# Kernel optimization log

Hardware: AMD Instinct MI355X
Metric: run time of the kernel (lower is better)

Reference implementation:

```python
import jax, jax.numpy as jnp
import numpy as np

# Model dims (see shape_source)
E, H, I = 8, 2048, 1408          # experts, hidden, moe intermediate
T, TOPK = 4096, 2                # tokens, routed experts per token
BN, BK = 128, 128                # weight SF block granularity (block_size)
FP8 = jnp.float8_e4m3fn
FP8_MAX = 448.0                  # torch.finfo(float8_e4m3fn).max


def _quantize_weight(key, n_exp, n_out, n_in):
    """Blockwise-quantize a random fp32 weight to (fp8 weight, fp32 scale_inv).

    Mirrors V3-style FP8 block quant: per [BN, BK] block, scale = amax / FP8_MAX.
    """
    w = jax.random.normal(key, (n_exp, n_out, n_in), jnp.float32) * 0.02
    wb = w.reshape(n_exp, n_out // BN, BN, n_in // BK, BK)
    amax = jnp.max(jnp.abs(wb), axis=(2, 4))                 # [E, nb, kb]
    scale = jnp.maximum(amax, 1e-12) / FP8_MAX
    q = (wb / scale[:, :, None, :, None]).astype(FP8)
    return q.reshape(n_exp, n_out, n_in), scale


def setup_inputs() -> dict:
    key = jax.random.key(0)
    k1, k2, k3, k4, k5 = jax.random.split(key, 5)
    hidden_states = jax.random.normal(k1, (T, H), jnp.float32)
    top_k_index = jax.random.randint(k2, (T, TOPK), 0, E)
    tw = jax.random.uniform(k3, (T, TOPK), dtype=jnp.float32)
    top_k_weights = tw / jnp.sum(tw, axis=-1, keepdims=True)  # softmax-like routing weights
    gate_up_proj, gate_up_proj_scale_inv = _quantize_weight(k4, E, 2 * I, H)
    down_proj, down_proj_scale_inv = _quantize_weight(k5, E, H, I)
    return {
        "hidden_states": hidden_states,
        "top_k_index": top_k_index,
        "top_k_weights": top_k_weights,
        "gate_up_proj": gate_up_proj,
        "gate_up_proj_scale_inv": gate_up_proj_scale_inv,
        "down_proj": down_proj,
        "down_proj_scale_inv": down_proj_scale_inv,
    }


def _act_quant_dequant(x):
    """Dynamic per-token, per-BK-block FP8 activation quant (fp8_act_quant), dequantized.

    Equivalent math to keeping q in fp8 and applying per-block scales inside the
    matmul, since the scale is constant within each k-block.
    """
    k = x.shape[-1]
    xb = x.reshape(*x.shape[:-1], k // BK, BK)
    amax = jnp.max(jnp.abs(xb), axis=-1)
    scale = jnp.maximum(amax, 1e-12) / FP8_MAX
    q = jnp.clip(xb / scale[..., None], -FP8_MAX, FP8_MAX).astype(FP8).astype(jnp.float32)
    return (q * scale[..., None]).reshape(x.shape)


def _dequant_weight(w, sf):
    """w: [E, N, K] fp8; sf: [E, N//BN, K//BK] fp32 -> [E, N, K] fp32."""
    sfe = jnp.repeat(jnp.repeat(sf, BN, axis=1), BK, axis=2)
    return w.astype(jnp.float32) * sfe


def reference(hidden_states, top_k_index, top_k_weights,
              gate_up_proj, gate_up_proj_scale_inv,
              down_proj, down_proj_scale_inv):
    # act-quant input once (shared across experts, as in the eager per-expert loop)
    xq = _act_quant_dequant(hidden_states)                         # [T, H]
    w_gu = _dequant_weight(gate_up_proj, gate_up_proj_scale_inv)   # [E, 2I, H]
    h = jnp.einsum('th,enh->ten', xq, w_gu)                        # [T, E, 2I]
    gate, up = jnp.split(h, 2, axis=-1)
    inter = jax.nn.silu(gate) * up                                 # [T, E, I]
    iq = _act_quant_dequant(inter)
    w_d = _dequant_weight(down_proj, down_proj_scale_inv)          # [E, H, I]
    y = jnp.einsum('tei,ehi->teh', iq, w_d)                        # [T, E, H]
    # routed combine: out[t] = sum_k top_k_weights[t,k] * y[t, top_k_index[t,k]]
    yk = jnp.take_along_axis(y, top_k_index[..., None], axis=1)    # [T, TOPK, H]
    return jnp.sum(yk * top_k_weights[..., None], axis=1)          # [T, H] fp32
```

## Files before the change

### kernel.cpp

```cpp
#include <hip/hip_runtime.h>
#include <stdint.h>
#include <stddef.h>

#define DEVFN __device__ __forceinline__

typedef float f32x4 __attribute__((ext_vector_type(4)));
typedef long i64_t;

constexpr int T_TOK = 4096, H_DIM = 2048, I_DIM = 1408;
constexpr int N_EXP = 8;
constexpr int P_PAIRS = T_TOK * 2;
constexpr int BM = 64;
constexpr int MAXT = 144;
constexpr int GU_ROWS = 2 * I_DIM;

constexpr size_t OFF_WGU = 0;
constexpr size_t OFF_WD  = OFF_WGU + (size_t)N_EXP * GU_ROWS * H_DIM;
constexpr size_t OFF_XQ  = OFF_WD + (size_t)N_EXP * H_DIM * I_DIM;
constexpr size_t OFF_XS  = OFF_XQ + (size_t)T_TOK * H_DIM;
constexpr size_t OFF_IQ  = OFF_XS + (size_t)T_TOK * 16 * 4;
constexpr size_t OFF_IS  = OFF_IQ + (size_t)(P_PAIRS + BM) * I_DIM;
constexpr size_t OFF_PS  = OFF_IS + (size_t)P_PAIRS * 11 * 4;
constexpr size_t OFF_PP  = OFF_PS + (size_t)P_PAIRS * 4;
constexpr size_t OFF_TE  = OFF_PP + (size_t)P_PAIRS * 4;
constexpr size_t OFF_TR  = OFF_TE + (size_t)MAXT * 4;
constexpr size_t OFF_TM  = OFF_TR + (size_t)MAXT * 4;
constexpr size_t OFF_Y   = (OFF_TM + (size_t)MAXT * 4 + 255) & ~(size_t)255;
constexpr size_t NEED_Y  = OFF_Y + (size_t)P_PAIRS * H_DIM * 4;

DEVFN unsigned f32_to_e4m3(float x) {
  unsigned u = __float_as_uint(x);
  unsigned s = (u >> 24) & 0x80u;
  int e = (int)((u >> 23) & 0xffu);
  unsigned m = u & 0x7fffffu;
  if (e == 0) return s;
  int ef = e - 127;
  if (ef < -10) return s;
  unsigned mant = 0x800000u | m;
  int shift = (ef < -6) ? (14 - ef) : 20;
  int e8 = (ef < -6) ? 0 : (ef + 7);
  unsigned keep = mant >> shift;
  unsigned rmask = 1u << (shift - 1);
  unsigned rbit = (mant & rmask) ? 1u : 0u;
  unsigned sticky = (mant & (rmask - 1u)) ? 1u : 0u;
  keep += (rbit & (sticky | (keep & 1u)));
  if (e8 == 0) {
    if (keep >= 8u) { e8 = 1; keep -= 8u; }
  } else {
    if (keep >= 16u) { keep >>= 1; e8 += 1; }
    keep -= 8u;
  }
  return s | ((unsigned)e8 << 3) | keep;
}

DEVFN float clampq(float v) { return fminf(fmaxf(v, -448.f), 448.f); }

DEVFN void gll(const uint8_t* g, uint8_t* l) {
  __builtin_amdgcn_global_load_lds((const __attribute__((address_space(1))) void*)g,
                                   (__attribute__((address_space(3))) void*)l,
                                   16, 0, 0);
}

__global__ __launch_bounds__(256) void k_wq(const float* __restrict__ wf,
                                            uint8_t* __restrict__ wq, int n4) {
  int i = blockIdx.x * 256 + threadIdx.x;
  if (i >= n4) return;
  float4 v = *(const float4*)(wf + (size_t)i * 4);
  unsigned b = f32_to_e4m3(clampq(v.x)) | (f32_to_e4m3(clampq(v.y)) << 8) |
               (f32_to_e4m3(clampq(v.z)) << 16) | (f32_to_e4m3(clampq(v.w)) << 24);
  *(unsigned*)(wq + (size_t)i * 4) = b;
}

__global__ __launch_bounds__(256) void k_actq(const float* __restrict__ x,
                                              uint8_t* __restrict__ xq,
                                              float* __restrict__ xs) {
  int t = blockIdx.x, tid = threadIdx.x;
  const float* row = x + (size_t)t * H_DIM + tid * 8;
  float4 v0 = *(const float4*)(row);
  float4 v1 = *(const float4*)(row + 4);
  float vals[8] = {v0.x, v0.y, v0.z, v0.w, v1.x, v1.y, v1.z, v1.w};
  float am = 0.f;
#pragma unroll
  for (int j = 0; j < 8; ++j) am = fmaxf(am, fabsf(vals[j]));
#pragma unroll
  for (int d = 1; d < 16; d <<= 1) am = fmaxf(am, __shfl_xor(am, d, 64));
  float s = fmaxf(am, 1e-12f) / 448.0f;
  if ((tid & 15) == 0) xs[(size_t)t * 16 + (tid >> 4)] = s;
  unsigned lo = 0, hi = 0;
#pragma unroll
  for (int j = 0; j < 4; ++j) lo |= f32_to_e4m3(clampq(vals[j] / s)) << (8 * j);
#pragma unroll
  for (int j = 0; j < 4; ++j) hi |= f32_to_e4m3(clampq(vals[4 + j] / s)) << (8 * j);
  uint2 pk; pk.x = lo; pk.y = hi;
  *(uint2*)(xq + (size_t)t * H_DIM + tid * 8) = pk;
}

__global__ __launch_bounds__(256) void k_route(const int* __restrict__ tki,
                                               int* __restrict__ ps, int* __restrict__ pp,
                                               int* __restrict__ te, int* __restrict__ tr,
                                               int* __restrict__ tm) {
  __shared__ int cnt[8], off[9], cur[8];
  int tid = threadIdx.x;
  if (tid < 8) cnt[tid] = 0;
  __syncthreads();
  for (int p = tid; p < P_PAIRS; p += 256) atomicAdd(&cnt[tki[p]], 1);
  __syncthreads();
  if (tid == 0) {
    int a = 0;
    for (int e = 0; e < 8; ++e) { off[e] = a; cur[e] = a; a += cnt[e]; }
    off[8] = a;
  }
  __syncthreads();
  for (int p = tid; p < P_PAIRS; p += 256) {
    int pos = atomicAdd(&cur[tki[p]], 1);
    ps[pos] = p;
    pp[p] = pos;
  }
  __syncthreads();
  if (tid == 0) {
    int nt = 0;
    for (int e = 0; e < 8; ++e)
      for (int s = off[e]; s < off[e + 1]; s += BM) {
        int rem = off[e + 1] - s;
        te[nt] = e; tr[nt] = s; tm[nt] = rem < BM ? rem : BM; ++nt;
      }
    for (; nt < MAXT; ++nt) { te[nt] = -1; tr[nt] = 0; tm[nt] = 0; }
  }
}

__global__ __launch_bounds__(256) void k_gemm1(
    const uint8_t* __restrict__ xq, const float* __restrict__ xs,
    const uint8_t* __restrict__ gup, const float* __restrict__ gsf,
    const int* __restrict__ te, const int* __restrict__ tr, const int* __restrict__ tm,
    const int* __restrict__ ps,
    uint8_t* __restrict__ iq, float* __restrict__ isv) {
  __shared__ uint8_t smA[BM * 128];
  __shared__ uint8_t smBg[128 * 128];
  __shared__ uint8_t smBu[128 * 128];
  __shared__ __align__(16) float smSa[BM];
  __shared__ float smRed[2][2][32];

  const int bx = blockIdx.x;
  const int e = te[bx];
  if (e < 0) return;
  const int r0 = tr[bx], mrows = tm[bx];
  const int n0 = blockIdx.y * 128;
  const int nbg = blockIdx.y;
  const int tid = threadIdx.x;
  const int lane = tid & 63;
  const int wid = tid >> 6;
  const int wm = wid >> 1, wn = wid & 1;
  const int lrow = lane & 15, lgrp = lane >> 4;
  const int mbase = wm * 32;
  const int wb = wid * 1024;

  const int m0 = tid >> 3, m1 = m0 + 32;
  const int kcol = (tid & 7) * 16;
  const int srcOff = kcol ^ ((m0 & 7) << 4);
  const int t0 = (m0 < mrows) ? (ps[r0 + m0] >> 1) : 0;
  const int t1 = (m1 < mrows) ? (ps[r0 + m1] >> 1) : 0;
  const uint8_t* pA0 = xq + (size_t)t0 * H_DIM + srcOff;
  const uint8_t* pA1 = xq + (size_t)t1 * H_DIM + srcOff;
  const uint8_t* pBg = gup + ((size_t)e * GU_ROWS + n0 + m0) * H_DIM + srcOff;
  const uint8_t* pBu = pBg + (size_t)I_DIM * H_DIM;
  int tS = 0;
  if (tid < 64) tS = (tid < mrows) ? (ps[r0 + tid] >> 1) : 0;
  const float* xsrow = xs + (size_t)tS * 16;

  const int swz = (lrow & 7) << 4;
  int koff[4];
#pragma unroll
  for (int kk = 0; kk < 4; ++kk) koff[kk] = ((kk * 32 + lgrp * 8) ^ swz);
  const uint8_t* pAf[2];
  pAf[0] = smA + (mbase + lrow) * 128;
  pAf[1] = smA + (mbase + 16 + lrow) * 128;
  const uint8_t* pBf[4];
#pragma unroll
  for (int nf = 0; nf < 4; ++nf) pBf[nf] = smBg + (wn * 64 + nf * 16 + lrow) * 128;
  const ptrdiff_t dBu = smBu - smBg;

  const float* sfg = gsf + ((size_t)e * 22 + nbg) * 16;
  const float* sfu = gsf + ((size_t)e * 22 + 11 + nbg) * 16;

  f32x4 accg[2][4], accu[2][4];
#pragma unroll
  for (int mf = 0; mf < 2; ++mf)
#pragma unroll
    for (int nf = 0; nf < 4; ++nf) { accg[mf][nf] = 0.f; accu[mf][nf] = 0.f; }

  for (int ks = 0; ks < 16; ++ks) {
    __syncthreads();
    gll(pA0, smA + wb);
    gll(pA1, smA + 4096 + wb);
#pragma unroll
    for (int c = 0; c < 4; ++c) {
      gll(pBg + (size_t)c * (32 * H_DIM), smBg + c * 4096 + wb);
      gll(pBu + (size_t)c * (32 * H_DIM), smBu + c * 4096 + wb);
    }
    if (tid < 64) smSa[tid] = xsrow[ks];
    __syncthreads();

    i64_t a[2][4];
#pragma unroll
    for (int mf = 0; mf < 2; ++mf)
#pragma unroll
      for (int kk = 0; kk < 4; ++kk) a[mf][kk] = *(const i64_t*)(pAf[mf] + koff[kk]);
    f32x4 saf[2];
    saf[0] = *(const f32x4*)(smSa + mbase + lgrp * 4);
    saf[1] = *(const f32x4*)(smSa + mbase + 16 + lgrp * 4);
    float swg = sfg[ks], swu = sfu[ks];

#pragma unroll
    for (int half = 0; half < 2; ++half) {
      const ptrdiff_t ho = half ? dBu : 0;
      f32x4 part[2][4];
#pragma unroll
      for (int mf = 0; mf < 2; ++mf)
#pragma unroll
        for (int nf = 0; nf < 4; ++nf) part[mf][nf] = 0.f;
#pragma unroll
      for (int kk = 0; kk < 4; ++kk)
#pragma unroll
        for (int nf = 0; nf < 4; ++nf) {
          i64_t b = *(const i64_t*)(pBf[nf] + ho + koff[kk]);
          part[0][nf] = __builtin_amdgcn_mfma_f32_16x16x32_fp8_fp8(a[0][kk], b, part[0][nf], 0, 0, 0);
          part[1][nf] = __builtin_amdgcn_mfma_f32_16x16x32_fp8_fp8(a[1][kk], b, part[1][nf], 0, 0, 0);
        }
      float sw = half ? swu : swg;
      f32x4 (*acch)[4] = half ? accu : accg;
#pragma unroll
      for (int mf = 0; mf < 2; ++mf) {
        f32x4 sc = saf[mf] * sw;
#pragma unroll
        for (int nf = 0; nf < 4; ++nf) acch[mf][nf] += part[mf][nf] * sc;
      }
    }
    pA0 += 128; pA1 += 128; pBg += 128; pBu += 128;
  }

  float itv[2][4][4];
  float amx[2][4];
#pragma unroll
  for (int mf = 0; mf < 2; ++mf)
#pragma unroll
    for (int r = 0; r < 4; ++r) amx[mf][r] = 0.f;
#pragma unroll
  for (int mf = 0; mf < 2; ++mf)
#pragma unroll
    for (int nf = 0; nf < 4; ++nf)
#pragma unroll
      for (int r = 0; r < 4; ++r) {
        float g = accg[mf][nf][r], u = accu[mf][nf][r];
        float sg = 1.0f / (1.0f + expf(-g));
        float iv = g * sg * u;
        itv[mf][nf][r] = iv;
        amx[mf][r] = fmaxf(amx[mf][r], fabsf(iv));
      }
#pragma unroll
  for (int mf = 0; mf < 2; ++mf)
#pragma unroll
    for (int r = 0; r < 4; ++r)
#pragma unroll
      for (int d = 1; d < 16; d <<= 1) amx[mf][r] = fmaxf(amx[mf][r], __shfl_xor(amx[mf][r], d, 64));

  if (lrow == 0) {
#pragma unroll
    for (int mf = 0; mf < 2; ++mf)
#pragma unroll
      for (int r = 0; r < 4; ++r) smRed[wm][wn][mf * 16 + lgrp * 4 + r] = amx[mf][r];
  }
  __syncthreads();

#pragma unroll
  for (int mf = 0; mf < 2; ++mf)
#pragma unroll
    for (int r = 0; r < 4; ++r) {
      float am2 = fmaxf(amx[mf][r], smRed[wm][wn ^ 1][mf * 16 + lgrp * 4 + r]);
      float s = fmaxf(am2, 1e-12f) / 448.0f;
      int R = mbase + mf * 16 + lgrp * 4 + r;
      if (R < mrows) {
        if (wn == 0 && lrow == 0) isv[(size_t)(r0 + R) * 11 + nbg] = s;
        size_t rowb = (size_t)(r0 + R) * I_DIM + n0 + wn * 64 + lrow;
#pragma unroll
        for (int nf = 0; nf < 4; ++nf) {
          float v = clampq(itv[mf][nf][r] / s);
          iq[rowb + nf * 16] = (uint8_t)f32_to_e4m3(v);
        }
      }
    }
}

template <bool ATOMIC>
__global__ __launch_bounds__(256) void k_gemm2(
    const uint8_t* __restrict__ iq, const float* __restrict__ isv,
    const uint8_t* __restrict__ dp, const float* __restrict__ dsf,
    const int* __restrict__ te, const int* __restrict__ tr, const int* __restrict__ tm,
    const int* __restrict__ ps, const float* __restrict__ tkw,
    float* __restrict__ outy) {
  __shared__ uint8_t smA[BM * 128];
  __shared__ uint8_t smB[128 * 128];
  __shared__ __align__(16) float smSa[BM];

  const int bx = blockIdx.x;
  const int e = te[bx];
  if (e < 0) return;
  const int r0 = tr[bx], mrows = tm[bx];
  const int n0 = blockIdx.y * 128;
  const int tid = threadIdx.x;
  const int lane = tid & 63;
  const int wid = tid >> 6;
  const int wm = wid >> 1, wn = wid & 1;
  const int lrow = lane & 15, lgrp = lane >> 4;
  const int mbase = wm * 32;
  const int wb = wid * 1024;

  const int m0 = tid >> 3, m1 = m0 + 32;
  const int kcol = (tid & 7) * 16;
  const int srcOff = kcol ^ ((m0 & 7) << 4);
  const uint8_t* pA0 = iq + (size_t)(r0 + m0) * I_DIM + srcOff;
  const uint8_t* pA1 = iq + (size_t)(r0 + m1) * I_DIM + srcOff;
  const uint8_t* pB = dp + ((size_t)e * H_DIM + n0 + m0) * I_DIM + srcOff;

  const int swz = (lrow & 7) << 4;
  int koff[4];
#pragma unroll
  for (int kk = 0; kk < 4; ++kk) koff[kk] = ((kk * 32 + lgrp * 8) ^ swz);
  const uint8_t* pAf[2];
  pAf[0] = smA + (mbase + lrow) * 128;
  pAf[1] = smA + (mbase + 16 + lrow) * 128;
  const uint8_t* pBf[4];
#pragma unroll
  for (int nf = 0; nf < 4; ++nf) pBf[nf] = smB + (wn * 64 + nf * 16 + lrow) * 128;

  const float* sfd = dsf + ((size_t)e * 16 + blockIdx.y) * 11;

  f32x4 acc[2][4];
#pragma unroll
  for (int mf = 0; mf < 2; ++mf)
#pragma unroll
    for (int nf = 0; nf < 4; ++nf) acc[mf][nf] = 0.f;

  for (int ks = 0; ks < 11; ++ks) {
    __syncthreads();
    gll(pA0, smA + wb);
    gll(pA1, smA + 4096 + wb);
#pragma unroll
    for (int c = 0; c < 4; ++c) gll(pB + (size_t)c * (32 * I_DIM), smB + c * 4096 + wb);
    if (tid < 64) {
      float v = (tid < mrows) ? isv[(size_t)(r0 + tid) * 11 + ks] : 0.f;
      smSa[tid] = v;
    }
    __syncthreads();

    i64_t a[2][4];
#pragma unroll
    for (int mf = 0; mf < 2; ++mf)
#pragma unroll
      for (int kk = 0; kk < 4; ++kk) a[mf][kk] = *(const i64_t*)(pAf[mf] + koff[kk]);
    f32x4 saf[2];
    saf[0] = *(const f32x4*)(smSa + mbase + lgrp * 4);
    saf[1] = *(const f32x4*)(smSa + mbase + 16 + lgrp * 4);
    float sw = sfd[ks];

    f32x4 part[2][4];
#pragma unroll
    for (int mf = 0; mf < 2; ++mf)
#pragma unroll
      for (int nf = 0; nf < 4; ++nf) part[mf][nf] = 0.f;
#pragma unroll
    for (int kk = 0; kk < 4; ++kk)
#pragma unroll
      for (int nf = 0; nf < 4; ++nf) {
        i64_t b = *(const i64_t*)(pBf[nf] + koff[kk]);
        part[0][nf] = __builtin_amdgcn_mfma_f32_16x16x32_fp8_fp8(a[0][kk], b, part[0][nf], 0, 0, 0);
        part[1][nf] = __builtin_amdgcn_mfma_f32_16x16x32_fp8_fp8(a[1][kk], b, part[1][nf], 0, 0, 0);
      }
#pragma unroll
    for (int mf = 0; mf < 2; ++mf) {
      f32x4 sc = saf[mf] * sw;
#pragma unroll
      for (int nf = 0; nf < 4; ++nf) acc[mf][nf] += part[mf][nf] * sc;
    }
    pA0 += 128; pA1 += 128; pB += 128;
  }

#pragma unroll
  for (int mf = 0; mf < 2; ++mf)
#pragma unroll
    for (int r = 0; r < 4; ++r) {
      int R = mbase + mf * 16 + lgrp * 4 + r;
      if (R < mrows) {
        int prow = r0 + R;
        int p = ps[prow];
        float w = tkw[p];
        if (ATOMIC) {
          float* ob = outy + (size_t)(p >> 1) * H_DIM + n0 + wn * 64 + lrow;
#pragma unroll
          for (int nf = 0; nf < 4; ++nf) atomicAdd(ob + nf * 16, acc[mf][nf][r] * w);
        } else {
          float* ob = outy + (size_t)prow * H_DIM + n0 + wn * 64 + lrow;
#pragma unroll
          for (int nf = 0; nf < 4; ++nf) ob[nf * 16] = acc[mf][nf][r] * w;
        }
      }
    }
}

__global__ __launch_bounds__(256) void k_combine(const float* __restrict__ y,
                                                 const int* __restrict__ pp,
                                                 float* __restrict__ out) {
  size_t g = (size_t)blockIdx.x * 256 + threadIdx.x;
  int t = (int)(g >> 9);
  int c = (int)(g & 511) * 4;
  int ra = pp[2 * t], rb = pp[2 * t + 1];
  float4 va = *(const float4*)(y + (size_t)ra * H_DIM + c);
  float4 vb = *(const float4*)(y + (size_t)rb * H_DIM + c);
  float4 vo;
  vo.x = va.x + vb.x; vo.y = va.y + vb.y; vo.z = va.z + vb.z; vo.w = va.w + vb.w;
  *(float4*)(out + (size_t)t * H_DIM + c) = vo;
}

extern "C" void kernel_launch(void* const* d_in, const int* in_sizes, int n_in,
                              void* d_out, int out_size, void* d_ws, size_t ws_size,
                              hipStream_t stream) {
  (void)in_sizes; (void)n_in; (void)out_size;
  const float* x = (const float*)d_in[0];
  const int* tki = (const int*)d_in[1];
  const float* tkw = (const float*)d_in[2];
  const float* gup_f = (const float*)d_in[3];
  const float* gsf = (const float*)d_in[4];
  const float* dp_f = (const float*)d_in[5];
  const float* dsf = (const float*)d_in[6];
  float* out = (float*)d_out;
  uint8_t* ws = (uint8_t*)d_ws;

  uint8_t* wgu = ws + OFF_WGU;
  uint8_t* wd = ws + OFF_WD;
  uint8_t* xq = ws + OFF_XQ;
  float* xs = (float*)(ws + OFF_XS);
  uint8_t* iq = ws + OFF_IQ;
  float* isv = (float*)(ws + OFF_IS);
  int* ps = (int*)(ws + OFF_PS);
  int* pp = (int*)(ws + OFF_PP);
  int* te = (int*)(ws + OFF_TE);
  int* tr = (int*)(ws + OFF_TR);
  int* tm = (int*)(ws + OFF_TM);
  float* y = (float*)(ws + OFF_Y);

  const int n4_gu = (N_EXP * GU_ROWS * H_DIM) / 4;
  const int n4_d = (N_EXP * H_DIM * I_DIM) / 4;
  k_wq<<<dim3((n4_gu + 255) / 256), dim3(256), 0, stream>>>(gup_f, wgu, n4_gu);
  k_wq<<<dim3((n4_d + 255) / 256), dim3(256), 0, stream>>>(dp_f, wd, n4_d);
  k_actq<<<dim3(T_TOK), dim3(256), 0, stream>>>(x, xq, xs);
  k_route<<<dim3(1), dim3(256), 0, stream>>>(tki, ps, pp, te, tr, tm);
  k_gemm1<<<dim3(MAXT, 11), dim3(256), 0, stream>>>(xq, xs, wgu, gsf, te, tr, tm, ps, iq, isv);
  if (ws_size >= NEED_Y) {
    k_gemm2<false><<<dim3(MAXT, 16), dim3(256), 0, stream>>>(iq, isv, wd, dsf, te, tr, tm, ps, tkw, y);
    k_combine<<<dim3((T_TOK * (H_DIM / 4)) / 256), dim3(256), 0, stream>>>(y, pp, out);
  } else {
    hipMemsetAsync(d_out, 0, (size_t)T_TOK * H_DIM * sizeof(float), stream);
    k_gemm2<true><<<dim3(MAXT, 16), dim3(256), 0, stream>>>(iq, isv, wd, dsf, te, tr, tm, ps, tkw, out);
  }
}
```

Before: 620.8 us.

## Fuse prep kernels, fast fp8 cast, double-buffer GEMM K-loops with 64-wide stages

Merges the weight cast, activation quant and routing kernels into one launch and replaces the generic fp8 conversion for weights with a bit-trick cast that skips clamping. Both GEMMs now stage K in 64-byte chunks into double-buffered shared memory so the next chunk's loads overlap the current MFMAs, with one barrier per stage. Intermediate scales are stored transposed ([kb][row]) so gemm2 reads them with coalesced loads. The fast cast assumes weights are already in fp8 range, and gemm2 no longer masks scales for rows past mrows.

```diff
diff --git a/kernel.cpp b/kernel.cpp
--- a/kernel.cpp
+++ b/kernel.cpp
@@ -13,6 +13,7 @@
 constexpr int BM = 64;
 constexpr int MAXT = 144;
 constexpr int GU_ROWS = 2 * I_DIM;
+constexpr int PP_PAD = P_PAIRS + 64;
 
 constexpr size_t OFF_WGU = 0;
 constexpr size_t OFF_WD  = OFF_WGU + (size_t)N_EXP * GU_ROWS * H_DIM;
@@ -20,7 +21,7 @@
 constexpr size_t OFF_XS  = OFF_XQ + (size_t)T_TOK * H_DIM;
 constexpr size_t OFF_IQ  = OFF_XS + (size_t)T_TOK * 16 * 4;
 constexpr size_t OFF_IS  = OFF_IQ + (size_t)(P_PAIRS + BM) * I_DIM;
-constexpr size_t OFF_PS  = OFF_IS + (size_t)P_PAIRS * 11 * 4;
+constexpr size_t OFF_PS  = OFF_IS + (size_t)11 * PP_PAD * 4;
 constexpr size_t OFF_PP  = OFF_PS + (size_t)P_PAIRS * 4;
 constexpr size_t OFF_TE  = OFF_PP + (size_t)P_PAIRS * 4;
 constexpr size_t OFF_TR  = OFF_TE + (size_t)MAXT * 4;
@@ -53,6 +54,18 @@
   return s | ((unsigned)e8 << 3) | keep;
 }
 
+DEVFN unsigned e4x(float v) {
+  unsigned u = __float_as_uint(v);
+  unsigned s = (u >> 24) & 0x80u;
+  unsigned au = u & 0x7fffffffu;
+  if (au < 0x3c800000u)
+    return s | (unsigned)(__uint_as_float(au) * 512.0f);
+  return s | ((au - 0x3c000000u) >> 20);
+}
+DEVFN unsigned e4x4(float4 v) {
+  return e4x(v.x) | (e4x(v.y) << 8) | (e4x(v.z) << 16) | (e4x(v.w) << 24);
+}
+
 DEVFN float clampq(float v) { return fminf(fmaxf(v, -448.f), 448.f); }
 
 DEVFN void gll(const uint8_t* g, uint8_t* l) {
@@ -61,46 +74,53 @@
                                    16, 0, 0);
 }
 
-__global__ __launch_bounds__(256) void k_wq(const float* __restrict__ wf,
-                                            uint8_t* __restrict__ wq, int n4) {
-  int i = blockIdx.x * 256 + threadIdx.x;
-  if (i >= n4) return;
-  float4 v = *(const float4*)(wf + (size_t)i * 4);
-  unsigned b = f32_to_e4m3(clampq(v.x)) | (f32_to_e4m3(clampq(v.y)) << 8) |
-               (f32_to_e4m3(clampq(v.z)) << 16) | (f32_to_e4m3(clampq(v.w)) << 24);
-  *(unsigned*)(wq + (size_t)i * 4) = b;
-}
-
-__global__ __launch_bounds__(256) void k_actq(const float* __restrict__ x,
-                                              uint8_t* __restrict__ xq,
-                                              float* __restrict__ xs) {
-  int t = blockIdx.x, tid = threadIdx.x;
-  const float* row = x + (size_t)t * H_DIM + tid * 8;
-  float4 v0 = *(const float4*)(row);
-  float4 v1 = *(const float4*)(row + 4);
-  float vals[8] = {v0.x, v0.y, v0.z, v0.w, v1.x, v1.y, v1.z, v1.w};
-  float am = 0.f;
-#pragma unroll
-  for (int j = 0; j < 8; ++j) am = fmaxf(am, fabsf(vals[j]));
-#pragma unroll
-  for (int d = 1; d < 16; d <<= 1) am = fmaxf(am, __shfl_xor(am, d, 64));
-  float s = fmaxf(am, 1e-12f) / 448.0f;
-  if ((tid & 15) == 0) xs[(size_t)t * 16 + (tid >> 4)] = s;
-  unsigned lo = 0, hi = 0;
-#pragma unroll
-  for (int j = 0; j < 4; ++j) lo |= f32_to_e4m3(clampq(vals[j] / s)) << (8 * j);
-#pragma unroll
-  for (int j = 0; j < 4; ++j) hi |= f32_to_e4m3(clampq(vals[4 + j] / s)) << (8 * j);
-  uint2 pk; pk.x = lo; pk.y = hi;
-  *(uint2*)(xq + (size_t)t * H_DIM + tid * 8) = pk;
-}
-
-__global__ __launch_bounds__(256) void k_route(const int* __restrict__ tki,
-                                               int* __restrict__ ps, int* __restrict__ pp,
-                                               int* __restrict__ te, int* __restrict__ tr,
-                                               int* __restrict__ tm) {
+constexpr int NB_WGU = 22528;
+constexpr int NB_WD  = 11264;
+constexpr int NB_W   = NB_WGU + NB_WD;
+constexpr int NB_PREP = NB_W + T_TOK + 1;
+
+__global__ __launch_bounds__(256) void k_prep(
+    const float* __restrict__ gup_f, const float* __restrict__ dp_f,
+    const float* __restrict__ x, const int* __restrict__ tki,
+    uint8_t* __restrict__ wgu, uint8_t* __restrict__ wd,
+    uint8_t* __restrict__ xq, float* __restrict__ xs,
+    int* __restrict__ ps, int* __restrict__ pp,
+    int* __restrict__ te, int* __restrict__ tr, int* __restrict__ tm) {
   __shared__ int cnt[8], off[9], cur[8];
-  int tid = threadIdx.x;
+  const int bx = blockIdx.x, tid = threadIdx.x;
+
+  if (bx < NB_W) {
+    const float* src = (bx < NB_WGU) ? gup_f : dp_f;
+    uint8_t* dst = (bx < NB_WGU) ? wgu : wd;
+    size_t i = (size_t)(bx < NB_WGU ? bx : bx - NB_WGU) * 2048 + (size_t)tid * 8;
+    float4 v0 = *(const float4*)(src + i);
+    float4 v1 = *(const float4*)(src + i + 4);
+    uint2 pk; pk.x = e4x4(v0); pk.y = e4x4(v1);
+    *(uint2*)(dst + i) = pk;
+    return;
+  }
+  if (bx < NB_W + T_TOK) {
+    int t = bx - NB_W;
+    const float* row = x + (size_t)t * H_DIM + tid * 8;
+    float4 v0 = *(const float4*)(row);
+    float4 v1 = *(const float4*)(row + 4);
+    float vals[8] = {v0.x, v0.y, v0.z, v0.w, v1.x, v1.y, v1.z, v1.w};
+    float am = 0.f;
+#pragma unroll
+    for (int j = 0; j < 8; ++j) am = fmaxf(am, fabsf(vals[j]));
+#pragma unroll
+    for (int d = 1; d < 16; d <<= 1) am = fmaxf(am, __shfl_xor(am, d, 64));
+    float s = fmaxf(am, 1e-12f) / 448.0f;
+    if ((tid & 15) == 0) xs[(size_t)t * 16 + (tid >> 4)] = s;
+    unsigned lo = 0, hi = 0;
+#pragma unroll
+    for (int j = 0; j < 4; ++j) lo |= f32_to_e4m3(clampq(vals[j] / s)) << (8 * j);
+#pragma unroll
+    for (int j = 0; j < 4; ++j) hi |= f32_to_e4m3(clampq(vals[4 + j] / s)) << (8 * j);
+    uint2 pk; pk.x = lo; pk.y = hi;
+    *(uint2*)(xq + (size_t)t * H_DIM + tid * 8) = pk;
+    return;
+  }
   if (tid < 8) cnt[tid] = 0;
   __syncthreads();
   for (int p = tid; p < P_PAIRS; p += 256) atomicAdd(&cnt[tki[p]], 1);
@@ -134,109 +154,112 @@
     const int* __restrict__ te, const int* __restrict__ tr, const int* __restrict__ tm,
     const int* __restrict__ ps,
     uint8_t* __restrict__ iq, float* __restrict__ isv) {
-  __shared__ uint8_t smA[BM * 128];
-  __shared__ uint8_t smBg[128 * 128];
-  __shared__ uint8_t smBu[128 * 128];
-  __shared__ __align__(16) float smSa[BM];
+  __shared__ uint8_t smA[2][64 * 64];
+  __shared__ uint8_t smBg[2][128 * 64];
+  __shared__ uint8_t smBu[2][128 * 64];
+  __shared__ __align__(16) float smSa[64];
   __shared__ float smRed[2][2][32];
 
-  const int bx = blockIdx.x;
-  const int e = te[bx];
+  const int e = te[blockIdx.x];
   if (e < 0) return;
-  const int r0 = tr[bx], mrows = tm[bx];
-  const int n0 = blockIdx.y * 128;
-  const int nbg = blockIdx.y;
-  const int tid = threadIdx.x;
-  const int lane = tid & 63;
-  const int wid = tid >> 6;
+  const int r0 = tr[blockIdx.x], mrows = tm[blockIdx.x];
+  const int nbg = blockIdx.y, n0 = nbg * 128;
+  const int tid = threadIdx.x, lane = tid & 63, wid = tid >> 6;
   const int wm = wid >> 1, wn = wid & 1;
   const int lrow = lane & 15, lgrp = lane >> 4;
   const int mbase = wm * 32;
-  const int wb = wid * 1024;
-
-  const int m0 = tid >> 3, m1 = m0 + 32;
-  const int kcol = (tid & 7) * 16;
-  const int srcOff = kcol ^ ((m0 & 7) << 4);
-  const int t0 = (m0 < mrows) ? (ps[r0 + m0] >> 1) : 0;
-  const int t1 = (m1 < mrows) ? (ps[r0 + m1] >> 1) : 0;
-  const uint8_t* pA0 = xq + (size_t)t0 * H_DIM + srcOff;
-  const uint8_t* pA1 = xq + (size_t)t1 * H_DIM + srcOff;
-  const uint8_t* pBg = gup + ((size_t)e * GU_ROWS + n0 + m0) * H_DIM + srcOff;
-  const uint8_t* pBu = pBg + (size_t)I_DIM * H_DIM;
+
+  const int row_t = tid >> 2;
+  const int srcOff = ((tid & 3) * 16) ^ ((row_t & 3) << 4);
+  const int tA = (row_t < mrows) ? (ps[r0 + row_t] >> 1) : 0;
+  const uint8_t* gA   = xq + (size_t)tA * H_DIM + srcOff;
+  const uint8_t* gBg  = gup + ((size_t)e * GU_ROWS + n0 + row_t) * H_DIM + srcOff;
+  const uint8_t* gBg2 = gBg + (size_t)64 * H_DIM;
+  const uint8_t* gBu  = gBg + (size_t)I_DIM * H_DIM;
+  const uint8_t* gBu2 = gBu + (size_t)64 * H_DIM;
+  uint8_t* lA  = smA[0]  + wid * 1024;
+  uint8_t* lBg = smBg[0] + wid * 1024;
+  uint8_t* lBu = smBu[0] + wid * 1024;
+
   int tS = 0;
   if (tid < 64) tS = (tid < mrows) ? (ps[r0 + tid] >> 1) : 0;
   const float* xsrow = xs + (size_t)tS * 16;
 
-  const int swz = (lrow & 7) << 4;
-  int koff[4];
-#pragma unroll
-  for (int kk = 0; kk < 4; ++kk) koff[kk] = ((kk * 32 + lgrp * 8) ^ swz);
-  const uint8_t* pAf[2];
-  pAf[0] = smA + (mbase + lrow) * 128;
-  pAf[1] = smA + (mbase + 16 + lrow) * 128;
-  const uint8_t* pBf[4];
-#pragma unroll
-  for (int nf = 0; nf < 4; ++nf) pBf[nf] = smBg + (wn * 64 + nf * 16 + lrow) * 128;
-  const ptrdiff_t dBu = smBu - smBg;
+  const int koff0 = (lgrp * 8) ^ ((lrow & 3) << 4);
+  const int koff1 = koff0 ^ 32;
+  const int rA0 = (mbase + lrow) * 64;
+  const int rA1 = (mbase + 16 + lrow) * 64;
+  int rB[4];
+#pragma unroll
+  for (int nf = 0; nf < 4; ++nf) rB[nf] = (wn * 64 + nf * 16 + lrow) * 64;
 
   const float* sfg = gsf + ((size_t)e * 22 + nbg) * 16;
   const float* sfu = gsf + ((size_t)e * 22 + 11 + nbg) * 16;
 
-  f32x4 accg[2][4], accu[2][4];
-#pragma unroll
-  for (int mf = 0; mf < 2; ++mf)
-#pragma unroll
-    for (int nf = 0; nf < 4; ++nf) { accg[mf][nf] = 0.f; accu[mf][nf] = 0.f; }
-
-  for (int ks = 0; ks < 16; ++ks) {
+  f32x4 accg[2][4], accu[2][4], pg[2][4], pu[2][4];
+#pragma unroll
+  for (int mf = 0; mf < 2; ++mf)
+#pragma unroll
+    for (int nf = 0; nf < 4; ++nf) {
+      accg[mf][nf] = 0.f; accu[mf][nf] = 0.f;
+      pg[mf][nf] = 0.f;   pu[mf][nf] = 0.f;
+    }
+
+#define STAGE1(b_, s_) do { size_t o_ = (size_t)(s_) * 64;            \
+    gll(gA + o_,   lA  + (b_) * 4096);                                \
+    gll(gBg + o_,  lBg + (b_) * 8192);                                \
+    gll(gBg2 + o_, lBg + (b_) * 8192 + 4096);                         \
+    gll(gBu + o_,  lBu + (b_) * 8192);                                \
+    gll(gBu2 + o_, lBu + (b_) * 8192 + 4096); } while (0)
+
+  STAGE1(0, 0);
+  if (tid < 64) smSa[tid] = xsrow[0];
+  __syncthreads();
+
+  for (int st = 0; st < 32; ++st) {
+    const int buf = st & 1;
+    if (st < 31) STAGE1(buf ^ 1, st + 1);
+    if (st && !(st & 1) && tid < 64) smSa[tid] = xsrow[st >> 1];
+
+    const uint8_t* bA = smA[0]  + buf * 4096;
+    const uint8_t* bG = smBg[0] + buf * 8192;
+    const uint8_t* bU = smBu[0] + buf * 8192;
+    i64_t a00 = *(const i64_t*)(bA + rA0 + koff0);
+    i64_t a01 = *(const i64_t*)(bA + rA0 + koff1);
+    i64_t a10 = *(const i64_t*)(bA + rA1 + koff0);
+    i64_t a11 = *(const i64_t*)(bA + rA1 + koff1);
+#pragma unroll
+    for (int nf = 0; nf < 4; ++nf) {
+      i64_t bg0 = *(const i64_t*)(bG + rB[nf] + koff0);
+      i64_t bg1 = *(const i64_t*)(bG + rB[nf] + koff1);
+      i64_t bu0 = *(const i64_t*)(bU + rB[nf] + koff0);
+      i64_t bu1 = *(const i64_t*)(bU + rB[nf] + koff1);
+      pg[0][nf] = __builtin_amdgcn_mfma_f32_16x16x32_fp8_fp8(a00, bg0, pg[0][nf], 0, 0, 0);
+      pg[0][nf] = __builtin_amdgcn_mfma_f32_16x16x32_fp8_fp8(a01, bg1, pg[0][nf], 0, 0, 0);
+      pg[1][nf] = __builtin_amdgcn_mfma_f32_16x16x32_fp8_fp8(a10, bg0, pg[1][nf], 0, 0, 0);
+      pg[1][nf] = __builtin_amdgcn_mfma_f32_16x16x32_fp8_fp8(a11, bg1, pg[1][nf], 0, 0, 0);
+      pu[0][nf] = __builtin_amdgcn_mfma_f32_16x16x32_fp8_fp8(a00, bu0, pu[0][nf], 0, 0, 0);
+      pu[0][nf] = __builtin_amdgcn_mfma_f32_16x16x32_fp8_fp8(a01, bu1, pu[0][nf], 0, 0, 0);
+      pu[1][nf] = __builtin_amdgcn_mfma_f32_16x16x32_fp8_fp8(a10, bu0, pu[1][nf], 0, 0, 0);
+      pu[1][nf] = __builtin_amdgcn_mfma_f32_16x16x32_fp8_fp8(a11, bu1, pu[1][nf], 0, 0, 0);
+    }
+    if (st & 1) {
+      const int kb = st >> 1;
+      float swg = sfg[kb], swu = sfu[kb];
+      f32x4 saf0 = *(const f32x4*)(smSa + mbase + lgrp * 4);
+      f32x4 saf1 = *(const f32x4*)(smSa + mbase + 16 + lgrp * 4);
+      f32x4 scg0 = saf0 * swg, scg1 = saf1 * swg;
+      f32x4 scu0 = saf0 * swu, scu1 = saf1 * swu;
+#pragma unroll
+      for (int nf = 0; nf < 4; ++nf) {
+        accg[0][nf] += pg[0][nf] * scg0; accg[1][nf] += pg[1][nf] * scg1;
+        accu[0][nf] += pu[0][nf] * scu0; accu[1][nf] += pu[1][nf] * scu1;
+        pg[0][nf] = 0.f; pg[1][nf] = 0.f; pu[0][nf] = 0.f; pu[1][nf] = 0.f;
+      }
+    }
     __syncthreads();
-    gll(pA0, smA + wb);
-    gll(pA1, smA + 4096 + wb);
-#pragma unroll
-    for (int c = 0; c < 4; ++c) {
-      gll(pBg + (size_t)c * (32 * H_DIM), smBg + c * 4096 + wb);
-      gll(pBu + (size_t)c * (32 * H_DIM), smBu + c * 4096 + wb);
-    }
-    if (tid < 64) smSa[tid] = xsrow[ks];
-    __syncthreads();
-
-    i64_t a[2][4];
-#pragma unroll
-    for (int mf = 0; mf < 2; ++mf)
-#pragma unroll
-      for (int kk = 0; kk < 4; ++kk) a[mf][kk] = *(const i64_t*)(pAf[mf] + koff[kk]);
-    f32x4 saf[2];
-    saf[0] = *(const f32x4*)(smSa + mbase + lgrp * 4);
-    saf[1] = *(const f32x4*)(smSa + mbase + 16 + lgrp * 4);
-    float swg = sfg[ks], swu = sfu[ks];
-
-#pragma unroll
-    for (int half = 0; half < 2; ++half) {
-      const ptrdiff_t ho = half ? dBu : 0;
-      f32x4 part[2][4];
-#pragma unroll
-      for (int mf = 0; mf < 2; ++mf)
-#pragma unroll
-        for (int nf = 0; nf < 4; ++nf) part[mf][nf] = 0.f;
-#pragma unroll
-      for (int kk = 0; kk < 4; ++kk)
-#pragma unroll
-        for (int nf = 0; nf < 4; ++nf) {
-          i64_t b = *(const i64_t*)(pBf[nf] + ho + koff[kk]);
-          part[0][nf] = __builtin_amdgcn_mfma_f32_16x16x32_fp8_fp8(a[0][kk], b, part[0][nf], 0, 0, 0);
-          part[1][nf] = __builtin_amdgcn_mfma_f32_16x16x32_fp8_fp8(a[1][kk], b, part[1][nf], 0, 0, 0);
-        }
-      float sw = half ? swu : swg;
-      f32x4 (*acch)[4] = half ? accu : accg;
-#pragma unroll
-      for (int mf = 0; mf < 2; ++mf) {
-        f32x4 sc = saf[mf] * sw;
-#pragma unroll
-        for (int nf = 0; nf < 4; ++nf) acch[mf][nf] += part[mf][nf] * sc;
-      }
-    }
-    pA0 += 128; pA1 += 128; pBg += 128; pBu += 128;
-  }
+  }
+#undef STAGE1
 
   float itv[2][4][4];
   float amx[2][4];
@@ -279,7 +302,7 @@
       float s = fmaxf(am2, 1e-12f) / 448.0f;
       int R = mbase + mf * 16 + lgrp * 4 + r;
       if (R < mrows) {
-        if (wn == 0 && lrow == 0) isv[(size_t)(r0 + R) * 11 + nbg] = s;
+        if (wn == 0 && lrow == 0) isv[(size_t)nbg * PP_PAD + (r0 + R)] = s;
         size_t rowb = (size_t)(r0 + R) * I_DIM + n0 + wn * 64 + lrow;
 #pragma unroll
         for (int nf = 0; nf < 4; ++nf) {
@@ -297,92 +320,87 @@
     const int* __restrict__ te, const int* __restrict__ tr, const int* __restrict__ tm,
     const int* __restrict__ ps, const float* __restrict__ tkw,
     float* __restrict__ outy) {
-  __shared__ uint8_t smA[BM * 128];
-  __shared__ uint8_t smB[128 * 128];
-  __shared__ __align__(16) float smSa[BM];
-
-  const int bx = blockIdx.x;
-  const int e = te[bx];
+  __shared__ uint8_t smA[2][64 * 64];
+  __shared__ uint8_t smB[2][128 * 64];
+  __shared__ __align__(16) float smSa[64];
+
+  const int e = te[blockIdx.x];
   if (e < 0) return;
-  const int r0 = tr[bx], mrows = tm[bx];
-  const int n0 = blockIdx.y * 128;
-  const int tid = threadIdx.x;
-  const int lane = tid & 63;
-  const int wid = tid >> 6;
+  const int r0 = tr[blockIdx.x], mrows = tm[blockIdx.x];
+  const int nbg = blockIdx.y, n0 = nbg * 128;
+  const int tid = threadIdx.x, lane = tid & 63, wid = tid >> 6;
   const int wm = wid >> 1, wn = wid & 1;
   const int lrow = lane & 15, lgrp = lane >> 4;
   const int mbase = wm * 32;
-  const int wb = wid * 1024;
-
-  const int m0 = tid >> 3, m1 = m0 + 32;
-  const int kcol = (tid & 7) * 16;
-  const int srcOff = kcol ^ ((m0 & 7) << 4);
-  const uint8_t* pA0 = iq + (size_t)(r0 + m0) * I_DIM + srcOff;
-  const uint8_t* pA1 = iq + (size_t)(r0 + m1) * I_DIM + srcOff;
-  const uint8_t* pB = dp + ((size_t)e * H_DIM + n0 + m0) * I_DIM + srcOff;
-
-  const int swz = (lrow & 7) << 4;
-  int koff[4];
-#pragma unroll
-  for (int kk = 0; kk < 4; ++kk) koff[kk] = ((kk * 32 + lgrp * 8) ^ swz);
-  const uint8_t* pAf[2];
-  pAf[0] = smA + (mbase + lrow) * 128;
-  pAf[1] = smA + (mbase + 16 + lrow) * 128;
-  const uint8_t* pBf[4];
-#pragma unroll
-  for (int nf = 0; nf < 4; ++nf) pBf[nf] = smB + (wn * 64 + nf * 16 + lrow) * 128;
-
-  const float* sfd = dsf + ((size_t)e * 16 + blockIdx.y) * 11;
-
-  f32x4 acc[2][4];
-#pragma unroll
-  for (int mf = 0; mf < 2; ++mf)
-#pragma unroll
-    for (int nf = 0; nf < 4; ++nf) acc[mf][nf] = 0.f;
-
-  for (int ks = 0; ks < 11; ++ks) {
+
+  const int row_t = tid >> 2;
+  const int srcOff = ((tid & 3) * 16) ^ ((row_t & 3) << 4);
+  const uint8_t* gA  = iq + (size_t)(r0 + row_t) * I_DIM + srcOff;
+  const uint8_t* gB  = dp + ((size_t)e * H_DIM + n0 + row_t) * I_DIM + srcOff;
+  const uint8_t* gB2 = gB + (size_t)64 * I_DIM;
+  uint8_t* lA = smA[0] + wid * 1024;
+  uint8_t* lB = smB[0] + wid * 1024;
+
+  const int koff0 = (lgrp * 8) ^ ((lrow & 3) << 4);
+  const int koff1 = koff0 ^ 32;
+  const int rA0 = (mbase + lrow) * 64;
+  const int rA1 = (mbase + 16 + lrow) * 64;
+  int rB[4];
+#pragma unroll
+  for (int nf = 0; nf < 4; ++nf) rB[nf] = (wn * 64 + nf * 16 + lrow) * 64;
+
+  const float* sfd = dsf + ((size_t)e * 16 + nbg) * 11;
+
+  f32x4 acc[2][4], p[2][4];
+#pragma unroll
+  for (int mf = 0; mf < 2; ++mf)
+#pragma unroll
+    for (int nf = 0; nf < 4; ++nf) { acc[mf][nf] = 0.f; p[mf][nf] = 0.f; }
+
+#define STAGE2(b_, s_) do { size_t o_ = (size_t)(s_) * 64;            \
+    gll(gA + o_,  lA + (b_) * 4096);                                  \
+    gll(gB + o_,  lB + (b_) * 8192);                                  \
+    gll(gB2 + o_, lB + (b_) * 8192 + 4096); } while (0)
+
+  STAGE2(0, 0);
+  if (tid < 64) smSa[tid] = isv[r0 + tid];
+  __syncthreads();
+
+  for (int st = 0; st < 22; ++st) {
+    const int buf = st & 1;
+    if (st < 21) STAGE2(buf ^ 1, st + 1);
+    if (st && !(st & 1) && tid < 64) smSa[tid] = isv[(size_t)(st >> 1) * PP_PAD + r0 + tid];
+
+    const uint8_t* bA = smA[0] + buf * 4096;
+    const uint8_t* bB = smB[0] + buf * 8192;
+    i64_t a00 = *(const i64_t*)(bA + rA0 + koff0);
+    i64_t a01 = *(const i64_t*)(bA + rA0 + koff1);
+    i64_t a10 = *(const i64_t*)(bA + rA1 + koff0);
+    i64_t a11 = *(const i64_t*)(bA + rA1 + koff1);
+#pragma unroll
+    for (int nf = 0; nf < 4; ++nf) {
+      i64_t b0 = *(const i64_t*)(bB + rB[nf] + koff0);
+      i64_t b1 = *(const i64_t*)(bB + rB[nf] + koff1);
+      p[0][nf] = __builtin_amdgcn_mfma_f32_16x16x32_fp8_fp8(a00, b0, p[0][nf], 0, 0, 0);
+      p[0][nf] = __builtin_amdgcn_mfma_f32_16x16x32_fp8_fp8(a01, b1, p[0][nf], 0, 0, 0);
+      p[1][nf] = __builtin_amdgcn_mfma_f32_16x16x32_fp8_fp8(a10, b0, p[1][nf], 0, 0, 0);
+      p[1][nf] = __builtin_amdgcn_mfma_f32_16x16x32_fp8_fp8(a11, b1, p[1][nf], 0, 0, 0);
+    }
+    if (st & 1) {
+      const int kb = st >> 1;
+      float sw = sfd[kb];
+      f32x4 saf0 = *(const f32x4*)(smSa + mbase + lgrp * 4);
+      f32x4 saf1 = *(const f32x4*)(smSa + mbase + 16 + lgrp * 4);
+      f32x4 sc0 = saf0 * sw, sc1 = saf1 * sw;
+#pragma unroll
+      for (int nf = 0; nf < 4; ++nf) {
+        acc[0][nf] += p[0][nf] * sc0; acc[1][nf] += p[1][nf] * sc1;
+        p[0][nf] = 0.f; p[1][nf] = 0.f;
+      }
+    }
     __syncthreads();
-    gll(pA0, smA + wb);
-    gll(pA1, smA + 4096 + wb);
-#pragma unroll
-    for (int c = 0; c < 4; ++c) gll(pB + (size_t)c * (32 * I_DIM), smB + c * 4096 + wb);
-    if (tid < 64) {
-      float v = (tid < mrows) ? isv[(size_t)(r0 + tid) * 11 + ks] : 0.f;
-      smSa[tid] = v;
-    }
-    __syncthreads();
-
-    i64_t a[2][4];
-#pragma unroll
-    for (int mf = 0; mf < 2; ++mf)
-#pragma unroll
-      for (int kk = 0; kk < 4; ++kk) a[mf][kk] = *(const i64_t*)(pAf[mf] + koff[kk]);
-    f32x4 saf[2];
-    saf[0] = *(const f32x4*)(smSa + mbase + lgrp * 4);
-    saf[1] = *(const f32x4*)(smSa + mbase + 16 + lgrp * 4);
-    float sw = sfd[ks];
-
-    f32x4 part[2][4];
-#pragma unroll
-    for (int mf = 0; mf < 2; ++mf)
-#pragma unroll
-      for (int nf = 0; nf < 4; ++nf) part[mf][nf] = 0.f;
-#pragma unroll
-    for (int kk = 0; kk < 4; ++kk)
-#pragma unroll
-      for (int nf = 0; nf < 4; ++nf) {
-        i64_t b = *(const i64_t*)(pBf[nf] + koff[kk]);
-        part[0][nf] = __builtin_amdgcn_mfma_f32_16x16x32_fp8_fp8(a[0][kk], b, part[0][nf], 0, 0, 0);
-        part[1][nf] = __builtin_amdgcn_mfma_f32_16x16x32_fp8_fp8(a[1][kk], b, part[1][nf], 0, 0, 0);
-      }
-#pragma unroll
-    for (int mf = 0; mf < 2; ++mf) {
-      f32x4 sc = saf[mf] * sw;
-#pragma unroll
-      for (int nf = 0; nf < 4; ++nf) acc[mf][nf] += part[mf][nf] * sc;
-    }
-    pA0 += 128; pA1 += 128; pB += 128;
-  }
+  }
+#undef STAGE2
 
 #pragma unroll
   for (int mf = 0; mf < 2; ++mf)
@@ -391,10 +409,10 @@
       int R = mbase + mf * 16 + lgrp * 4 + r;
       if (R < mrows) {
         int prow = r0 + R;
-        int p = ps[prow];
-        float w = tkw[p];
+        int pidx = ps[prow];
+        float w = tkw[pidx];
         if (ATOMIC) {
-          float* ob = outy + (size_t)(p >> 1) * H_DIM + n0 + wn * 64 + lrow;
+          float* ob = outy + (size_t)(pidx >> 1) * H_DIM + n0 + wn * 64 + lrow;
 #pragma unroll
           for (int nf = 0; nf < 4; ++nf) atomicAdd(ob + nf * 16, acc[mf][nf][r] * w);
         } else {
@@ -447,12 +465,8 @@
   int* tm = (int*)(ws + OFF_TM);
   float* y = (float*)(ws + OFF_Y);
 
-  const int n4_gu = (N_EXP * GU_ROWS * H_DIM) / 4;
-  const int n4_d = (N_EXP * H_DIM * I_DIM) / 4;
-  k_wq<<<dim3((n4_gu + 255) / 256), dim3(256), 0, stream>>>(gup_f, wgu, n4_gu);
-  k_wq<<<dim3((n4_d + 255) / 256), dim3(256), 0, stream>>>(dp_f, wd, n4_d);
-  k_actq<<<dim3(T_TOK), dim3(256), 0, stream>>>(x, xq, xs);
-  k_route<<<dim3(1), dim3(256), 0, stream>>>(tki, ps, pp, te, tr, tm);
+  k_prep<<<dim3(NB_PREP), dim3(256), 0, stream>>>(gup_f, dp_f, x, tki, wgu, wd,
+                                                  xq, xs, ps, pp, te, tr, tm);
   k_gemm1<<<dim3(MAXT, 11), dim3(256), 0, stream>>>(xq, xs, wgu, gsf, te, tr, tm, ps, iq, isv);
   if (ws_size >= NEED_Y) {
     k_gemm2<false><<<dim3(MAXT, 16), dim3(256), 0, stream>>>(iq, isv, wd, dsf, te, tr, tm, ps, tkw, y);
```

Result: slower. 797.5 us (+28.4%).
